# Kernel optimization log

Measured on AMD Instinct MI355X. Metric: run time of the kernel, lower is better.

The kernel has to match this reference:

```python
import jax, jax.numpy as jnp
import numpy as np

M = 16384      # total flat points per role (8 scenes x 2048 pts)
D = 256        # d_model
H = 4          # heads
K = 16         # knn neighbors
DFF = 1024     # 4*D
LN_EPS = 1e-5


def _ln(x, g, b):
    m = jnp.mean(x, axis=-1, keepdims=True)
    v = jnp.mean((x - m) ** 2, axis=-1, keepdims=True)
    return (x - m) / jnp.sqrt(v + LN_EPS) * g + b


def _knn_block(x, coord, ctx, ctx_coord, idx,
               Wq, Wk, Wv, Wo, g1, b1, pe_w, pe_b,
               W1, bf1, W2, bf2, g2, b2):
    # x: [M,D] query feats; ctx: [N,D] context feats; idx: [M,K] neighbor ids (-1 = invalid)
    m, d = x.shape
    k = idx.shape[1]
    dh = d // H
    valid = idx >= 0
    idx_c = jnp.where(valid, idx, 0)

    xn = _ln(x, g1, b1)
    q = (xn @ Wq).reshape(m, H, dh)                      # [M,H,dh]
    k_all = ctx @ Wk                                     # [N,D]
    v_all = ctx @ Wv                                     # [N,D]

    rel = coord[:, None, :] - ctx_coord[idx_c]           # [M,K,3]
    pe = rel @ pe_w + pe_b                               # [M,K,D] relative position encoding
    kg = (k_all[idx_c] + pe).reshape(m, k, H, dh)        # gathered keys  [M,K,H,dh]
    vg = (v_all[idx_c] + pe).reshape(m, k, H, dh)        # gathered values

    scale = jnp.asarray(1.0 / np.sqrt(dh), x.dtype)
    scores = jnp.einsum('mhd,mkhd->mhk', q, kg) * scale
    scores = jnp.where(valid[:, None, :], scores, jnp.asarray(-1e9, x.dtype))
    attn = jax.nn.softmax(scores, axis=-1)
    out = jnp.einsum('mhk,mkhd->mhd', attn, vg).reshape(m, d) @ Wo
    x = x + out
    h = jax.nn.gelu(_ln(x, g2, b2) @ W1 + bf1)
    return x + (h @ W2 + bf2)


def setup_inputs() -> dict:
    key = jax.random.key(0)
    ks = jax.random.split(key, 24)
    s = 0.02
    nblk = 2  # [0]=self(a), [1]=cross(a,b)
    inp = {
        'feat_a': jax.random.normal(ks[0], (M, D), jnp.float32),
        'coord_a': jax.random.normal(ks[1], (M, 3), jnp.float32),
        'feat_b': jax.random.normal(ks[2], (M, D), jnp.float32),
        'coord_b': jax.random.normal(ks[3], (M, 3), jnp.float32),
        'Wq': jax.random.normal(ks[4], (nblk, D, D), jnp.float32) * s,
        'Wk': jax.random.normal(ks[5], (nblk, D, D), jnp.float32) * s,
        'Wv': jax.random.normal(ks[6], (nblk, D, D), jnp.float32) * s,
        'Wo': jax.random.normal(ks[7], (nblk, D, D), jnp.float32) * s,
        'ln1_g': jnp.ones((nblk, D), jnp.float32),
        'ln1_b': jnp.zeros((nblk, D), jnp.float32),
        'pe_w': jax.random.normal(ks[8], (nblk, 3, D), jnp.float32) * s,
        'pe_b': jnp.zeros((nblk, D), jnp.float32),
        'ffn_w1': jax.random.normal(ks[9], (nblk, D, DFF), jnp.float32) * s,
        'ffn_b1': jnp.zeros((nblk, DFF), jnp.float32),
        'ffn_w2': jax.random.normal(ks[10], (nblk, DFF, D), jnp.float32) * s,
        'ffn_b2': jnp.zeros((nblk, D), jnp.float32),
        'ln2_g': jnp.ones((nblk, D), jnp.float32),
        'ln2_b': jnp.zeros((nblk, D), jnp.float32),
        'knn_a2a': jax.random.randint(ks[11], (M, K), 0, M, jnp.int64 if jax.config.jax_enable_x64 else jnp.int32),
        'knn_a2b': jax.random.randint(ks[12], (M, K), 0, M, jnp.int64 if jax.config.jax_enable_x64 else jnp.int32),
    }
    return inp


def reference(feat_a, coord_a, feat_b, coord_b,
              Wq, Wk, Wv, Wo, ln1_g, ln1_b, pe_w, pe_b,
              ffn_w1, ffn_b1, ffn_w2, ffn_b2, ln2_g, ln2_b,
              knn_a2a, knn_a2b):
    def params(i):
        return (Wq[i], Wk[i], Wv[i], Wo[i], ln1_g[i], ln1_b[i], pe_w[i], pe_b[i],
                ffn_w1[i], ffn_b1[i], ffn_w2[i], ffn_b2[i], ln2_g[i], ln2_b[i])
    # layer 'self(a)': feat[a] = block(feat[a], coord[a], knn_indexes['a2a'])
    fa = _knn_block(feat_a, coord_a, feat_a, coord_a, knn_a2a, *params(0))
    # layer 'cross(a,b)': feat[a] = block(query=feat[a], context=feat[b], knn_indexes['a2b'])
    fa = _knn_block(fa, coord_a, feat_b, coord_b, knn_a2b, *params(1))
    return fa
```

## Files before the change

kernel.cpp:

```cpp
#include <hip/hip_runtime.h>
#include <hip/hip_bf16.h>
#include <stdint.h>

#define MM 16384
#define DD 256
#define HH 4
#define KK 16
#define DFF_ 1024

typedef __attribute__((ext_vector_type(8))) short bf16x8;
typedef __attribute__((ext_vector_type(16))) float f32x16;
typedef __attribute__((ext_vector_type(2))) float f32x2;

__device__ __forceinline__ unsigned short f2bf(float f) {
    unsigned u = __builtin_bit_cast(unsigned, f);
    unsigned r = u + 0x7fffu + ((u >> 16) & 1u);
    return (unsigned short)(r >> 16);
}
__device__ __forceinline__ float bf2f(unsigned short h) {
    unsigned u = ((unsigned)h) << 16;
    return __builtin_bit_cast(float, u);
}


__global__ __launch_bounds__(256) void prep_weights(
        const float* __restrict__ Wq, const float* __restrict__ Wk,
        const float* __restrict__ Wv, const float* __restrict__ Wo,
        const float* __restrict__ W1, const float* __restrict__ W2,
        unsigned short* __restrict__ wf) {
    int t = blockIdx.x * blockDim.x + threadIdx.x;
    const float* src; unsigned short* dst;
    int kd, lg, rem, blk, e, sect;
    if (t < 131072) { sect = 0; rem = t; blk = rem >> 16; e = rem & 65535;
        src = Wq; dst = wf + blk * 65536; kd = 256; lg = 8; }
    else if (t < 262144) { sect = 1; rem = t - 131072; blk = rem >> 16; e = rem & 65535;
        src = Wk; dst = wf + 131072 + blk * 131072; kd = 256; lg = 8; }
    else if (t < 393216) { sect = 2; rem = t - 262144; blk = rem >> 16; e = rem & 65535;
        src = Wv; dst = wf + 131072 + blk * 131072; kd = 256; lg = 8; }
    else if (t < 524288) { sect = 0; rem = t - 393216; blk = rem >> 16; e = rem & 65535;
        src = Wo; dst = wf + 393216 + blk * 65536; kd = 256; lg = 8; }
    else if (t < 1048576) { sect = 0; rem = t - 524288; blk = rem >> 18; e = rem & 262143;
        src = W1; dst = wf + 524288 + blk * 262144; kd = 256; lg = 10; }
    else if (t < 1572864) { sect = 0; rem = t - 1048576; blk = rem >> 18; e = rem & 262143;
        src = W2; dst = wf + 1048576 + blk * 262144; kd = 1024; lg = 8; }
    else return;
    int k = e >> lg;
    int n = e & ((1 << lg) - 1);
    if (sect == 1) n = (n >> 2) * 8 + (n & 3);
    else if (sect == 2) n = (n >> 2) * 8 + 4 + (n & 3);
    float v = src[(size_t)blk * kd * (1 << lg) + e];
    int off = ((n >> 5) * (kd >> 4) + (k >> 4)) * 512 + (((k >> 3) & 1) * 32 + (n & 31)) * 8 + (k & 7);
    dst[off] = f2bf(v);
}

__global__ __launch_bounds__(256) void ln3_to_frag(
        const float* __restrict__ xa, const float* __restrict__ g,
        const float* __restrict__ b, const float* __restrict__ xb,
        unsigned short* __restrict__ outln, unsigned short* __restrict__ outca,
        unsigned short* __restrict__ outcb) {
    int y = blockIdx.y;
    const float* x = (y == 2) ? xb : xa;
    unsigned short* out = (y == 0) ? outln : (y == 1 ? outca : outcb);
    int apply_ln = (y == 0);
    int wave = threadIdx.x >> 6, lane = threadIdx.x & 63;
    int m = blockIdx.x * 4 + wave;
    const float4 xv = reinterpret_cast<const float4*>(x + (size_t)m * DD)[lane];
    float vals[4] = {xv.x, xv.y, xv.z, xv.w};
    int k0 = lane * 4;
    if (apply_ln) {
        float s = vals[0] + vals[1] + vals[2] + vals[3];
        float sq = vals[0]*vals[0] + vals[1]*vals[1] + vals[2]*vals[2] + vals[3]*vals[3];
        for (int o = 32; o; o >>= 1) { s += __shfl_xor(s, o, 64); sq += __shfl_xor(sq, o, 64); }
        float mean = s * (1.0f / DD);
        float var = sq * (1.0f / DD) - mean * mean;
        float rs = rsqrtf(var + 1e-5f);
        #pragma unroll
        for (int c = 0; c < 4; ++c)
            vals[c] = (vals[c] - mean) * rs * g[k0 + c] + b[k0 + c];
    }
    int chunk = ((m >> 5) * (DD >> 4) + (k0 >> 4)) * 64 + ((k0 >> 3) & 1) * 32 + (m & 31);
    ushort4 o4 = make_ushort4(f2bf(vals[0]), f2bf(vals[1]), f2bf(vals[2]), f2bf(vals[3]));
    *reinterpret_cast<ushort4*>(out + (size_t)chunk * 8 + (k0 & 7)) = o4;
}

constexpr int GOUT_F32 = 0;
constexpr int GOUT_GELU_FRAG = 2;

template <int KG>
__device__ __forceinline__ void compute_tile(
        const bf16x8* __restrict__ a0, const bf16x8* __restrict__ a1,
        const bf16x8* __restrict__ b0, const bf16x8* __restrict__ b1,
        f32x16 acc[2][2]) {
    #pragma unroll 4
    for (int g = 0; g < KG; ++g) {
        bf16x8 av0 = a0[g * 64];
        bf16x8 av1 = a1[g * 64];
        bf16x8 bv0 = b0[g * 64];
        bf16x8 bv1 = b1[g * 64];
        acc[0][0] = __builtin_amdgcn_mfma_f32_32x32x16_bf16(av0, bv0, acc[0][0], 0, 0, 0);
        acc[0][1] = __builtin_amdgcn_mfma_f32_32x32x16_bf16(av0, bv1, acc[0][1], 0, 0, 0);
        acc[1][0] = __builtin_amdgcn_mfma_f32_32x32x16_bf16(av1, bv0, acc[1][0], 0, 0, 0);
        acc[1][1] = __builtin_amdgcn_mfma_f32_32x32x16_bf16(av1, bv1, acc[1][1], 0, 0, 0);
    }
}

template <int KD, int NOUT, int MODE, bool RESID, bool BIAS>
__global__ __launch_bounds__(256) void gemm_frag(
        const bf16x8* __restrict__ A, const bf16x8* __restrict__ B,
        void* __restrict__ outp, const float* __restrict__ resid,
        const float* __restrict__ bias, int out_kd) {
    constexpr int KG = KD / 16;
    __shared__ float lds[MODE == GOUT_GELU_FRAG ? 4 * 1056 : 4];
    int wave = threadIdx.x >> 6, lane = threadIdx.x & 63;
    int wm = wave & 1, wn = wave >> 1;
    int m0 = blockIdx.x * 128 + wm * 64;
    int n0 = blockIdx.y * 128 + wn * 64;
    const bf16x8* a0 = A + ((size_t)(m0 >> 5) * KG) * 64 + lane;
    const bf16x8* a1 = a0 + (size_t)KG * 64;
    const bf16x8* b0 = B + ((size_t)(n0 >> 5) * KG) * 64 + lane;
    const bf16x8* b1 = b0 + (size_t)KG * 64;
    f32x16 acc[2][2] = {};
    compute_tile<KG>(a0, a1, b0, b1, acc);
    int col = lane & 31, rq = (lane >> 5) * 4;
    if constexpr (MODE == GOUT_F32) {
        #pragma unroll
        for (int i = 0; i < 2; ++i)
        #pragma unroll
        for (int j = 0; j < 2; ++j) {
            #pragma unroll
            for (int r = 0; r < 16; ++r) {
                int row = (r & 3) + 8 * (r >> 2) + rq;
                int m = m0 + i * 32 + row;
                int n = n0 + j * 32 + col;
                float v = acc[i][j][r];
                if (BIAS) v += bias[n];
                if (RESID) v += resid[(size_t)m * NOUT + n];
                ((float*)outp)[(size_t)m * NOUT + n] = v;
            }
        }
    } else {
        float* wlds = &lds[wave * 1056];
        for (int i = 0; i < 2; ++i)
        for (int j = 0; j < 2; ++j) {
            #pragma unroll
            for (int r = 0; r < 16; ++r) {
                int row = (r & 3) + 8 * (r >> 2) + rq;
                int n = n0 + j * 32 + col;
                float v = acc[i][j][r] + bias[n];
                float arg = v * (1.5957691216f + 0.0713548163f * v * v);
                v = v * __frcp_rn(1.0f + __expf(-arg));
                wlds[row * 33 + col] = v;
            }
            #pragma unroll
            for (int it = 0; it < 2; ++it) {
                int task = lane + it * 64;
                int row = task >> 2, cc = task & 3;
                int m = m0 + i * 32 + row;
                int k = n0 + j * 32 + cc * 8;
                float* p = &wlds[row * 33 + cc * 8];
                unsigned short us[8];
                #pragma unroll
                for (int e = 0; e < 8; ++e) us[e] = f2bf(p[e]);
                int chunk = ((m >> 5) * (out_kd >> 4) + (k >> 4)) * 64 + ((k >> 3) & 1) * 32 + (m & 31);
                reinterpret_cast<uint4*>(outp)[chunk] = *reinterpret_cast<uint4*>(us);
            }
        }
    }
}

template <int O, int N>
__device__ __forceinline__ void redstage(float* a, int lane) {
    int sel = lane & O;
    #pragma unroll
    for (int u = 0; u < N / 2; ++u) {
        float lo = a[2 * u], hi = a[2 * u + 1];
        float keep = sel ? hi : lo;
        float send = sel ? lo : hi;
        a[u] = keep + __shfl_xor(send, O, 64);
    }
}

template <int KD, bool BIAS>
__global__ __launch_bounds__(256) void gemm_ln(
        const bf16x8* __restrict__ A, const bf16x8* __restrict__ B,
        float* __restrict__ out_f32, const float* __restrict__ resid,
        const float* __restrict__ bias,
        const float* __restrict__ lng, const float* __restrict__ lnb,
        unsigned short* __restrict__ out_frag) {
    constexpr int KG = KD / 16;
    __shared__ float pstat[4][64][2];
    __shared__ float stats[64][2];
    __shared__ float tlds[4][32 * 33];
    int wave = threadIdx.x >> 6, lane = threadIdx.x & 63;
    int wn = wave;
    int m0 = blockIdx.x * 64;
    int n0 = wn * 64;
    const bf16x8* a0 = A + ((size_t)(m0 >> 5) * KG) * 64 + lane;
    const bf16x8* a1 = a0 + (size_t)KG * 64;
    const bf16x8* b0 = B + ((size_t)(n0 >> 5) * KG) * 64 + lane;
    const bf16x8* b1 = b0 + (size_t)KG * 64;
    f32x16 acc[2][2] = {};
    compute_tile<KG>(a0, a1, b0, b1, acc);
    int col = lane & 31, rq = (lane >> 5) * 4;

    #pragma unroll
    for (int i = 0; i < 2; ++i)
    #pragma unroll
    for (int j = 0; j < 2; ++j) {
        #pragma unroll
        for (int r = 0; r < 16; ++r) {
            int row = (r & 3) + 8 * (r >> 2) + rq;
            int m = m0 + i * 32 + row;
            int n = n0 + j * 32 + col;
            float v = acc[i][j][r];
            if (BIAS) v += bias[n];
            v += resid[(size_t)m * DD + n];
            out_f32[(size_t)m * DD + n] = v;
            acc[i][j][r] = v;
        }
    }

    {
        float ps[32];
        #pragma unroll
        for (int i = 0; i < 2; ++i)
        #pragma unroll
        for (int r = 0; r < 16; ++r)
            ps[i * 16 + r] = acc[i][0][r] + acc[i][1][r];
        redstage<1, 32>(ps, lane);
        redstage<2, 16>(ps, lane);
        redstage<4, 8>(ps, lane);
        redstage<8, 4>(ps, lane);
        redstage<16, 2>(ps, lane);
        float sum64 = ps[0];
        float qs[32];
        #pragma unroll
        for (int i = 0; i < 2; ++i)
        #pragma unroll
        for (int r = 0; r < 16; ++r) {
            float a = acc[i][0][r], b = acc[i][1][r];
            qs[i * 16 + r] = a * a + b * b;
        }
        redstage<1, 32>(qs, lane);
        redstage<2, 16>(qs, lane);
        redstage<4, 8>(qs, lane);
        redstage<8, 4>(qs, lane);
        redstage<16, 2>(qs, lane);
        float sq64 = qs[0];
        int slot = lane & 31;
        int ROW = (slot >> 4) * 32 + (slot & 3) + 8 * ((slot >> 2) & 3) + rq;
        *reinterpret_cast<float2*>(&pstat[wn][ROW][0]) = make_float2(sum64, sq64);
    }
    __syncthreads();
    if (threadIdx.x < 64) {
        int R = threadIdx.x;
        float s = 0.0f, sq = 0.0f;
        #pragma unroll
        for (int w = 0; w < 4; ++w) {
            float2 p = *reinterpret_cast<float2*>(&pstat[w][R][0]);
            s += p.x; sq += p.y;
        }
        float mean = s * (1.0f / DD);
        float var = sq * (1.0f / DD) - mean * mean;
        float rstd = rsqrtf(var + 1e-5f);
        *reinterpret_cast<float2*>(&stats[R][0]) = make_float2(mean, rstd);
    }
    __syncthreads();

    float* wlds = &tlds[wave][0];
    #pragma unroll
    for (int i = 0; i < 2; ++i) {
        float mean_r[16], rstd_r[16];
        #pragma unroll
        for (int r = 0; r < 16; ++r) {
            int row = (r & 3) + 8 * (r >> 2) + rq;
            float2 st = *reinterpret_cast<float2*>(&stats[i * 32 + row][0]);
            mean_r[r] = st.x; rstd_r[r] = st.y;
        }
        for (int j = 0; j < 2; ++j) {
            float gj = lng[n0 + j * 32 + col];
            float bj = lnb[n0 + j * 32 + col];
            #pragma unroll
            for (int r = 0; r < 16; ++r) {
                int row = (r & 3) + 8 * (r >> 2) + rq;
                float v = (acc[i][j][r] - mean_r[r]) * rstd_r[r] * gj + bj;
                wlds[row * 33 + col] = v;
            }
            #pragma unroll
            for (int it = 0; it < 2; ++it) {
                int task = lane + it * 64;
                int row = task >> 2, cc = task & 3;
                int m = m0 + i * 32 + row;
                int k = n0 + j * 32 + cc * 8;
                float* p = &wlds[row * 33 + cc * 8];
                unsigned short us[8];
                #pragma unroll
                for (int e = 0; e < 8; ++e) us[e] = f2bf(p[e]);
                int chunk = ((m >> 5) * (DD >> 4) + (k >> 4)) * 64 + ((k >> 3) & 1) * 32 + (m & 31);
                *reinterpret_cast<uint4*>(out_frag + (size_t)chunk * 8) = *reinterpret_cast<uint4*>(us);
            }
        }
    }
}

__global__ __launch_bounds__(256) void gemm_qkv(
        const bf16x8* __restrict__ Aq, const bf16x8* __restrict__ Akv,
        const bf16x8* __restrict__ Bq, const bf16x8* __restrict__ Bkv,
        unsigned short* __restrict__ qout, unsigned char* __restrict__ kvout) {
    constexpr int KG = 16;
    int wave = threadIdx.x >> 6, lane = threadIdx.x & 63;
    int wm = wave & 1, wn = wave >> 1;
    int y = blockIdx.y;
    bool isQ = y < 2;
    const bf16x8* A = isQ ? Aq : Akv;
    const bf16x8* B = isQ ? Bq : Bkv;
    int n0 = (isQ ? y : y - 2) * 128 + wn * 64;
    int m0 = blockIdx.x * 128 + wm * 64;
    const bf16x8* a0 = A + ((size_t)(m0 >> 5) * KG) * 64 + lane;
    const bf16x8* a1 = a0 + (size_t)KG * 64;
    const bf16x8* b0 = B + ((size_t)(n0 >> 5) * KG) * 64 + lane;
    const bf16x8* b1 = b0 + (size_t)KG * 64;
    f32x16 acc[2][2] = {};
    compute_tile<KG>(a0, a1, b0, b1, acc);
    int col = lane & 31, rq = (lane >> 5) * 4;
    #pragma unroll
    for (int i = 0; i < 2; ++i)
    #pragma unroll
    for (int j = 0; j < 2; ++j)
    #pragma unroll
    for (int r = 0; r < 16; ++r) {
        int row = (r & 3) + 8 * (r >> 2) + rq;
        int m = m0 + i * 32 + row;
        int n = n0 + j * 32 + col;
        float v = acc[i][j][r];
        if (isQ) qout[(size_t)m * 256 + n] = f2bf(v);
        else kvout[(size_t)m * 512 + n] =
            (unsigned char)(__builtin_amdgcn_cvt_pk_fp8_f32(v, v, 0, false) & 0xff);
    }
}

__global__ __launch_bounds__(256) void attn_kernel(
        const unsigned short* __restrict__ q, const unsigned char* __restrict__ kv,
        const float* __restrict__ coord, const float* __restrict__ ctx_coord,
        const int* __restrict__ knn,
        const float* __restrict__ pe_w, const float* __restrict__ pe_b,
        unsigned short* __restrict__ out_frag) {
    int wave = threadIdx.x >> 6, lane = threadIdx.x & 63;
    int m = blockIdx.x * 4 + wave;
    int s = lane & 15;
    int d0 = (lane >> 4) * 64 + s * 4;

    ushort4 qv4 = *reinterpret_cast<const ushort4*>(q + (size_t)m * DD + d0);
    float qx = bf2f(qv4.x), qy = bf2f(qv4.y), qz = bf2f(qv4.z), qw = bf2f(qv4.w);
    float4 pw0 = *reinterpret_cast<const float4*>(pe_w + d0);
    float4 pw1 = *reinterpret_cast<const float4*>(pe_w + DD + d0);
    float4 pw2 = *reinterpret_cast<const float4*>(pe_w + 2 * DD + d0);
    float4 pbv = *reinterpret_cast<const float4*>(pe_b + d0);

    float cx = coord[m * 3], cy = coord[m * 3 + 1], cz = coord[m * 3 + 2];
    int myidx = knn[(size_t)m * KK + s];
    int icm = myidx < 0 ? 0 : myidx;
    float rx = cx - ctx_coord[icm * 3];
    float ry = cy - ctx_coord[icm * 3 + 1];
    float rz = cz - ctx_coord[icm * 3 + 2];

    float t0 = qx * pw0.x + qy * pw0.y + qz * pw0.z + qw * pw0.w;
    float t1 = qx * pw1.x + qy * pw1.y + qz * pw1.z + qw * pw1.w;
    float t2 = qx * pw2.x + qy * pw2.y + qz * pw2.z + qw * pw2.w;
    float t3 = qx * pbv.x + qy * pbv.y + qz * pbv.z + qw * pbv.w;
    #pragma unroll
    for (int o = 1; o < 16; o <<= 1) {
        t0 += __shfl_xor(t0, o, 64);
        t1 += __shfl_xor(t1, o, 64);
        t2 += __shfl_xor(t2, o, 64);
        t3 += __shfl_xor(t3, o, 64);
    }

    float sc_own = 0.0f;
    unsigned vpk[KK];
    #pragma unroll
    for (int j = 0; j < KK; ++j) {
        int ij = __shfl(myidx, j, 64);
        int ic = ij < 0 ? 0 : ij;
        uint2 kvv = *reinterpret_cast<const uint2*>(kv + (size_t)ic * 512 + (d0 >> 2) * 8);
        vpk[j] = kvv.y;
        f32x2 k01 = __builtin_amdgcn_cvt_pk_f32_fp8(kvv.x, false);
        f32x2 k23 = __builtin_amdgcn_cvt_pk_f32_fp8(kvv.x, true);
        float p = qx * k01.x + qy * k01.y + qz * k23.x + qw * k23.y;
        p += __shfl_xor(p, 1, 64);
        p += __shfl_xor(p, 2, 64);
        p += __shfl_xor(p, 4, 64);
        p += __shfl_xor(p, 8, 64);
        sc_own = (j == s) ? p : sc_own;
    }
    float corr = rx * t0 + ry * t1 + rz * t2 + t3;
    sc_own = (myidx >= 0) ? (sc_own + corr) * 0.125f : -1e9f;

    float mx = sc_own;
    mx = fmaxf(mx, __shfl_xor(mx, 1, 64));
    mx = fmaxf(mx, __shfl_xor(mx, 2, 64));
    mx = fmaxf(mx, __shfl_xor(mx, 4, 64));
    mx = fmaxf(mx, __shfl_xor(mx, 8, 64));
    float e = __expf(sc_own - mx);
    float sum = e;
    sum += __shfl_xor(sum, 1, 64);
    sum += __shfl_xor(sum, 2, 64);
    sum += __shfl_xor(sum, 4, 64);
    sum += __shfl_xor(sum, 8, 64);
    float w_own = e * __frcp_rn(sum);

    float wrx = w_own * rx, wry = w_own * ry, wrz = w_own * rz;
    #pragma unroll
    for (int o = 1; o < 16; o <<= 1) {
        wrx += __shfl_xor(wrx, o, 64);
        wry += __shfl_xor(wry, o, 64);
        wrz += __shfl_xor(wrz, o, 64);
    }

    int gbase = lane & 48;
    float ax = 0.f, ay = 0.f, az = 0.f, aw = 0.f;
    #pragma unroll
    for (int j = 0; j < KK; ++j) {
        float wj = __shfl(w_own, gbase + j, 64);
        f32x2 v01 = __builtin_amdgcn_cvt_pk_f32_fp8(vpk[j], false);
        f32x2 v23 = __builtin_amdgcn_cvt_pk_f32_fp8(vpk[j], true);
        ax += wj * v01.x;
        ay += wj * v01.y;
        az += wj * v23.x;
        aw += wj * v23.y;
    }
    ax += wrx * pw0.x + wry * pw1.x + wrz * pw2.x + pbv.x;
    ay += wrx * pw0.y + wry * pw1.y + wrz * pw2.y + pbv.y;
    az += wrx * pw0.z + wry * pw1.z + wrz * pw2.z + pbv.z;
    aw += wrx * pw0.w + wry * pw1.w + wrz * pw2.w + pbv.w;

    ushort4 o4 = make_ushort4(f2bf(ax), f2bf(ay), f2bf(az), f2bf(aw));
    int chunk = ((m >> 5) * (DD >> 4) + (d0 >> 4)) * 64 + ((d0 >> 3) & 1) * 32 + (m & 31);
    *reinterpret_cast<ushort4*>(out_frag + (size_t)chunk * 8 + (d0 & 7)) = o4;
}

extern "C" void kernel_launch(void* const* d_in, const int* in_sizes, int n_in,
                              void* d_out, int out_size, void* d_ws, size_t ws_size,
                              hipStream_t stream) {
    const float* feat_a = (const float*)d_in[0];
    const float* coord_a = (const float*)d_in[1];
    const float* feat_b = (const float*)d_in[2];
    const float* coord_b = (const float*)d_in[3];
    const float* Wq = (const float*)d_in[4];
    const float* Wk = (const float*)d_in[5];
    const float* Wv = (const float*)d_in[6];
    const float* Wo = (const float*)d_in[7];
    const float* ln1_g = (const float*)d_in[8];
    const float* ln1_b = (const float*)d_in[9];
    const float* pe_w = (const float*)d_in[10];
    const float* pe_b = (const float*)d_in[11];
    const float* W1 = (const float*)d_in[12];
    const float* b1 = (const float*)d_in[13];
    const float* W2 = (const float*)d_in[14];
    const float* b2 = (const float*)d_in[15];
    const float* ln2_g = (const float*)d_in[16];
    const float* ln2_b = (const float*)d_in[17];
    const int* knn_a2a = (const int*)d_in[18];
    const int* knn_a2b = (const int*)d_in[19];

    char* ws = (char*)d_ws;
    unsigned short* wfrag = (unsigned short*)ws;
    float* xmid = (float*)(ws + (4ull << 20));
    float* xout0 = (float*)(ws + (20ull << 20));
    unsigned short* qbuf = (unsigned short*)(ws + (36ull << 20));
    unsigned char* kvbuf = (unsigned char*)(ws + (52ull << 20));
    unsigned short* xnf = (unsigned short*)(ws + (68ull << 20));
    unsigned short* ctxfa = (unsigned short*)(ws + (76ull << 20));
    unsigned short* attnf = (unsigned short*)(ws + (84ull << 20));
    unsigned short* ctxfb = (unsigned short*)(ws + (92ull << 20));
    unsigned short* geluf = (unsigned short*)(ws + (36ull << 20));

    const unsigned short* WQF = wfrag;
    const unsigned short* KVF = wfrag + 131072;
    const unsigned short* WOF = wfrag + 393216;
    const unsigned short* W1F = wfrag + 524288;
    const unsigned short* W2F = wfrag + 1048576;

    prep_weights<<<(1572864 + 255) / 256, 256, 0, stream>>>(Wq, Wk, Wv, Wo, W1, W2, wfrag);

    ln3_to_frag<<<dim3(MM / 4, 3), 256, 0, stream>>>(feat_a, ln1_g, ln1_b, feat_b,
                                                     xnf, ctxfa, ctxfb);

    gemm_qkv<<<dim3(MM / 128, 6), 256, 0, stream>>>(
        (const bf16x8*)xnf, (const bf16x8*)ctxfa,
        (const bf16x8*)WQF, (const bf16x8*)KVF, qbuf, kvbuf);

    attn_kernel<<<MM / 4, 256, 0, stream>>>(qbuf, kvbuf, coord_a, coord_a, knn_a2a,
                                            pe_w, pe_b, attnf);

    gemm_ln<256, false><<<MM / 64, 256, 0, stream>>>(
        (const bf16x8*)attnf, (const bf16x8*)WOF, xmid, feat_a, nullptr,
        ln2_g, ln2_b, xnf);

    gemm_frag<256, 1024, GOUT_GELU_FRAG, false, true><<<dim3(MM / 128, 8), 256, 0, stream>>>(
        (const bf16x8*)xnf, (const bf16x8*)W1F, geluf, nullptr, b1, 1024);

    gemm_ln<1024, true><<<MM / 64, 256, 0, stream>>>(
        (const bf16x8*)geluf, (const bf16x8*)W2F, xout0, xmid, b2,
        ln1_g + DD, ln1_b + DD, xnf);

    gemm_qkv<<<dim3(MM / 128, 6), 256, 0, stream>>>(
        (const bf16x8*)xnf, (const bf16x8*)ctxfb,
        (const bf16x8*)(WQF + 65536), (const bf16x8*)(KVF + 131072), qbuf, kvbuf);

    attn_kernel<<<MM / 4, 256, 0, stream>>>(qbuf, kvbuf, coord_a, coord_b, knn_a2b,
                                            pe_w + 3 * DD, pe_b + DD, attnf);

    gemm_ln<256, false><<<MM / 64, 256, 0, stream>>>(
        (const bf16x8*)attnf, (const bf16x8*)(WOF + 65536), xmid, xout0, nullptr,
        ln2_g + DD, ln2_b + DD, xnf);

    gemm_frag<256, 1024, GOUT_GELU_FRAG, false, true><<<dim3(MM / 128, 8), 256, 0, stream>>>(
        (const bf16x8*)xnf, (const bf16x8*)(W1F + 262144), geluf, nullptr,
        b1 + DFF_, 1024);

    gemm_frag<1024, 256, GOUT_F32, true, true><<<dim3(MM / 128, 2), 256, 0, stream>>>(
        (const bf16x8*)geluf, (const bf16x8*)(W2F + 262144), d_out, xmid,
        b2 + DD, 0);
}
```

Before: 335.7 us.

## Stage GEMM operand tiles into LDS via global_load_lds before MFMA

Replaces direct per-wave global fragment loads in the QKV, FFN1 and final FFN2 GEMMs with block-wide staging of A and B tiles into 128KB of shared memory using global_load_lds. The four waves then read shared data, so each global fragment is fetched once per block instead of once per wave. This removes duplicated global traffic, but the large LDS allocation limits occupancy to one block per CU. Load and compute are not overlapped within a chunk, since a full vmcnt wait and barrier come before each compute.

```diff
diff --git a/kernel.cpp b/kernel.cpp
--- a/kernel.cpp
+++ b/kernel.cpp
@@ -20,6 +20,12 @@
 __device__ __forceinline__ float bf2f(unsigned short h) {
     unsigned u = ((unsigned)h) << 16;
     return __builtin_bit_cast(float, u);
+}
+
+__device__ __forceinline__ void gload_lds16(const void* g, void* l) {
+    __builtin_amdgcn_global_load_lds(
+        (const __attribute__((address_space(1))) unsigned int*)g,
+        (__attribute__((address_space(3))) unsigned int*)l, 16, 0, 0);
 }
 
 
@@ -104,23 +110,53 @@
     }
 }
 
+template <int KG, int KGC>
+__device__ __forceinline__ void stage_tile(
+        const char* __restrict__ A, const char* __restrict__ B,
+        int m0, int n0, int c, char* smem, int wave, int lane) {
+    #pragma unroll
+    for (int r = 0; r < 32; ++r) {
+        int off = (wave + 4 * r) << 10;
+        const char* gsrc;
+        if (off < 65536) {
+            int grp = off >> 14, inner = off & 16383;
+            gsrc = A + (((size_t)((m0 >> 5) + grp) * KG + (size_t)c * KGC) << 10) + inner;
+        } else {
+            int o2 = off - 65536;
+            int grp = o2 >> 14, inner = o2 & 16383;
+            gsrc = B + (((size_t)((n0 >> 5) + grp) * KG + (size_t)c * KGC) << 10) + inner;
+        }
+        gload_lds16(gsrc + lane * 16, smem + off);
+    }
+}
+
 template <int KD, int NOUT, int MODE, bool RESID, bool BIAS>
-__global__ __launch_bounds__(256) void gemm_frag(
-        const bf16x8* __restrict__ A, const bf16x8* __restrict__ B,
+__global__ __launch_bounds__(256) void gemm_staged(
+        const char* __restrict__ A, const char* __restrict__ B,
         void* __restrict__ outp, const float* __restrict__ resid,
         const float* __restrict__ bias, int out_kd) {
     constexpr int KG = KD / 16;
-    __shared__ float lds[MODE == GOUT_GELU_FRAG ? 4 * 1056 : 4];
+    constexpr int KGC = 16;
+    constexpr int NCH = KG / KGC;
+    __shared__ char smem[131072];
     int wave = threadIdx.x >> 6, lane = threadIdx.x & 63;
     int wm = wave & 1, wn = wave >> 1;
-    int m0 = blockIdx.x * 128 + wm * 64;
-    int n0 = blockIdx.y * 128 + wn * 64;
-    const bf16x8* a0 = A + ((size_t)(m0 >> 5) * KG) * 64 + lane;
-    const bf16x8* a1 = a0 + (size_t)KG * 64;
-    const bf16x8* b0 = B + ((size_t)(n0 >> 5) * KG) * 64 + lane;
-    const bf16x8* b1 = b0 + (size_t)KG * 64;
+    int m0 = blockIdx.x * 128;
+    int n0 = blockIdx.y * 128;
+    const bf16x8* la0 = (const bf16x8*)smem + (2 * wm * KGC) * 64 + lane;
+    const bf16x8* la1 = la0 + KGC * 64;
+    const bf16x8* lb0 = (const bf16x8*)(smem + 65536) + (2 * wn * KGC) * 64 + lane;
+    const bf16x8* lb1 = lb0 + KGC * 64;
     f32x16 acc[2][2] = {};
-    compute_tile<KG>(a0, a1, b0, b1, acc);
+    #pragma unroll
+    for (int c = 0; c < NCH; ++c) {
+        if (c) __syncthreads();
+        stage_tile<KG, KGC>(A, B, m0, n0, c, smem, wave, lane);
+        asm volatile("s_waitcnt vmcnt(0)" ::: "memory");
+        __syncthreads();
+        compute_tile<KGC>(la0, la1, lb0, lb1, acc);
+    }
+    int mw = m0 + wm * 64, nw = n0 + wn * 64;
     int col = lane & 31, rq = (lane >> 5) * 4;
     if constexpr (MODE == GOUT_F32) {
         #pragma unroll
@@ -130,8 +166,8 @@
             #pragma unroll
             for (int r = 0; r < 16; ++r) {
                 int row = (r & 3) + 8 * (r >> 2) + rq;
-                int m = m0 + i * 32 + row;
-                int n = n0 + j * 32 + col;
+                int m = mw + i * 32 + row;
+                int n = nw + j * 32 + col;
                 float v = acc[i][j][r];
                 if (BIAS) v += bias[n];
                 if (RESID) v += resid[(size_t)m * NOUT + n];
@@ -139,13 +175,14 @@
             }
         }
     } else {
-        float* wlds = &lds[wave * 1056];
+        __syncthreads();
+        float* wlds = (float*)smem + wave * 1056;
         for (int i = 0; i < 2; ++i)
         for (int j = 0; j < 2; ++j) {
             #pragma unroll
             for (int r = 0; r < 16; ++r) {
                 int row = (r & 3) + 8 * (r >> 2) + rq;
-                int n = n0 + j * 32 + col;
+                int n = nw + j * 32 + col;
                 float v = acc[i][j][r] + bias[n];
                 float arg = v * (1.5957691216f + 0.0713548163f * v * v);
                 v = v * __frcp_rn(1.0f + __expf(-arg));
@@ -155,8 +192,8 @@
             for (int it = 0; it < 2; ++it) {
                 int task = lane + it * 64;
                 int row = task >> 2, cc = task & 3;
-                int m = m0 + i * 32 + row;
-                int k = n0 + j * 32 + cc * 8;
+                int m = mw + i * 32 + row;
+                int k = nw + j * 32 + cc * 8;
                 float* p = &wlds[row * 33 + cc * 8];
                 unsigned short us[8];
                 #pragma unroll
@@ -165,6 +202,47 @@
                 reinterpret_cast<uint4*>(outp)[chunk] = *reinterpret_cast<uint4*>(us);
             }
         }
+    }
+}
+
+__global__ __launch_bounds__(256) void gemm_qkv_st(
+        const char* __restrict__ Aq, const char* __restrict__ Akv,
+        const char* __restrict__ Bq, const char* __restrict__ Bkv,
+        unsigned short* __restrict__ qout, unsigned char* __restrict__ kvout) {
+    constexpr int KG = 16;
+    __shared__ char smem[131072];
+    int wave = threadIdx.x >> 6, lane = threadIdx.x & 63;
+    int wm = wave & 1, wn = wave >> 1;
+    int y = blockIdx.y;
+    bool isQ = y < 2;
+    const char* A = isQ ? Aq : Akv;
+    const char* B = isQ ? Bq : Bkv;
+    int m0 = blockIdx.x * 128;
+    int n0 = (isQ ? y : y - 2) * 128;
+    stage_tile<KG, KG>(A, B, m0, n0, 0, smem, wave, lane);
+    const bf16x8* la0 = (const bf16x8*)smem + (2 * wm * KG) * 64 + lane;
+    const bf16x8* la1 = la0 + KG * 64;
+    const bf16x8* lb0 = (const bf16x8*)(smem + 65536) + (2 * wn * KG) * 64 + lane;
+    const bf16x8* lb1 = lb0 + KG * 64;
+    f32x16 acc[2][2] = {};
+    asm volatile("s_waitcnt vmcnt(0)" ::: "memory");
+    __syncthreads();
+    compute_tile<KG>(la0, la1, lb0, lb1, acc);
+    int mw = m0 + wm * 64, nw = n0 + wn * 64;
+    int col = lane & 31, rq = (lane >> 5) * 4;
+    #pragma unroll
+    for (int i = 0; i < 2; ++i)
+    #pragma unroll
+    for (int j = 0; j < 2; ++j)
+    #pragma unroll
+    for (int r = 0; r < 16; ++r) {
+        int row = (r & 3) + 8 * (r >> 2) + rq;
+        int m = mw + i * 32 + row;
+        int n = nw + j * 32 + col;
+        float v = acc[i][j][r];
+        if (isQ) qout[(size_t)m * 256 + n] = f2bf(v);
+        else kvout[(size_t)m * 512 + n] =
+            (unsigned char)(__builtin_amdgcn_cvt_pk_fp8_f32(v, v, 0, false) & 0xff);
     }
 }
 
@@ -300,42 +378,6 @@
                 *reinterpret_cast<uint4*>(out_frag + (size_t)chunk * 8) = *reinterpret_cast<uint4*>(us);
             }
         }
-    }
-}
-
-__global__ __launch_bounds__(256) void gemm_qkv(
-        const bf16x8* __restrict__ Aq, const bf16x8* __restrict__ Akv,
-        const bf16x8* __restrict__ Bq, const bf16x8* __restrict__ Bkv,
-        unsigned short* __restrict__ qout, unsigned char* __restrict__ kvout) {
-    constexpr int KG = 16;
-    int wave = threadIdx.x >> 6, lane = threadIdx.x & 63;
-    int wm = wave & 1, wn = wave >> 1;
-    int y = blockIdx.y;
-    bool isQ = y < 2;
-    const bf16x8* A = isQ ? Aq : Akv;
-    const bf16x8* B = isQ ? Bq : Bkv;
-    int n0 = (isQ ? y : y - 2) * 128 + wn * 64;
-    int m0 = blockIdx.x * 128 + wm * 64;
-    const bf16x8* a0 = A + ((size_t)(m0 >> 5) * KG) * 64 + lane;
-    const bf16x8* a1 = a0 + (size_t)KG * 64;
-    const bf16x8* b0 = B + ((size_t)(n0 >> 5) * KG) * 64 + lane;
-    const bf16x8* b1 = b0 + (size_t)KG * 64;
-    f32x16 acc[2][2] = {};
-    compute_tile<KG>(a0, a1, b0, b1, acc);
-    int col = lane & 31, rq = (lane >> 5) * 4;
-    #pragma unroll
-    for (int i = 0; i < 2; ++i)
-    #pragma unroll
-    for (int j = 0; j < 2; ++j)
-    #pragma unroll
-    for (int r = 0; r < 16; ++r) {
-        int row = (r & 3) + 8 * (r >> 2) + rq;
-        int m = m0 + i * 32 + row;
-        int n = n0 + j * 32 + col;
-        float v = acc[i][j][r];
-        if (isQ) qout[(size_t)m * 256 + n] = f2bf(v);
-        else kvout[(size_t)m * 512 + n] =
-            (unsigned char)(__builtin_amdgcn_cvt_pk_fp8_f32(v, v, 0, false) & 0xff);
     }
 }
 
@@ -486,9 +528,9 @@
     ln3_to_frag<<<dim3(MM / 4, 3), 256, 0, stream>>>(feat_a, ln1_g, ln1_b, feat_b,
                                                      xnf, ctxfa, ctxfb);
 
-    gemm_qkv<<<dim3(MM / 128, 6), 256, 0, stream>>>(
-        (const bf16x8*)xnf, (const bf16x8*)ctxfa,
-        (const bf16x8*)WQF, (const bf16x8*)KVF, qbuf, kvbuf);
+    gemm_qkv_st<<<dim3(MM / 128, 6), 256, 0, stream>>>(
+        (const char*)xnf, (const char*)ctxfa,
+        (const char*)WQF, (const char*)KVF, qbuf, kvbuf);
 
     attn_kernel<<<MM / 4, 256, 0, stream>>>(qbuf, kvbuf, coord_a, coord_a, knn_a2a,
                                             pe_w, pe_b, attnf);
@@ -497,16 +539,16 @@
         (const bf16x8*)attnf, (const bf16x8*)WOF, xmid, feat_a, nullptr,
         ln2_g, ln2_b, xnf);
 
-    gemm_frag<256, 1024, GOUT_GELU_FRAG, false, true><<<dim3(MM / 128, 8), 256, 0, stream>>>(
-        (const bf16x8*)xnf, (const bf16x8*)W1F, geluf, nullptr, b1, 1024);
+    gemm_staged<256, 1024, GOUT_GELU_FRAG, false, true><<<dim3(MM / 128, 8), 256, 0, stream>>>(
+        (const char*)xnf, (const char*)W1F, geluf, nullptr, b1, 1024);
 
     gemm_ln<1024, true><<<MM / 64, 256, 0, stream>>>(
         (const bf16x8*)geluf, (const bf16x8*)W2F, xout0, xmid, b2,
         ln1_g + DD, ln1_b + DD, xnf);
 
-    gemm_qkv<<<dim3(MM / 128, 6), 256, 0, stream>>>(
-        (const bf16x8*)xnf, (const bf16x8*)ctxfb,
-        (const bf16x8*)(WQF + 65536), (const bf16x8*)(KVF + 131072), qbuf, kvbuf);
+    gemm_qkv_st<<<dim3(MM / 128, 6), 256, 0, stream>>>(
+        (const char*)xnf, (const char*)ctxfb,
+        (const char*)(WQF + 65536), (const char*)(KVF + 131072), qbuf, kvbuf);
 
     attn_kernel<<<MM / 4, 256, 0, stream>>>(qbuf, kvbuf, coord_a, coord_b, knn_a2b,
                                             pe_w + 3 * DD, pe_b + DD, attnf);
@@ -515,11 +557,11 @@
         (const bf16x8*)attnf, (const bf16x8*)(WOF + 65536), xmid, xout0, nullptr,
         ln2_g + DD, ln2_b + DD, xnf);
 
-    gemm_frag<256, 1024, GOUT_GELU_FRAG, false, true><<<dim3(MM / 128, 8), 256, 0, stream>>>(
-        (const bf16x8*)xnf, (const bf16x8*)(W1F + 262144), geluf, nullptr,
+    gemm_staged<256, 1024, GOUT_GELU_FRAG, false, true><<<dim3(MM / 128, 8), 256, 0, stream>>>(
+        (const char*)xnf, (const char*)(W1F + 262144), geluf, nullptr,
         b1 + DFF_, 1024);
 
-    gemm_frag<1024, 256, GOUT_F32, true, true><<<dim3(MM / 128, 2), 256, 0, stream>>>(
-        (const bf16x8*)geluf, (const bf16x8*)(W2F + 262144), d_out, xmid,
+    gemm_staged<1024, 256, GOUT_F32, true, true><<<dim3(MM / 128, 2), 256, 0, stream>>>(
+        (const char*)geluf, (const char*)(W2F + 262144), d_out, xmid,
         b2 + DD, 0);
 }
```

Measured after the change: 368.7 us. 1.1x slower.

## Split GEMM+LN tiles across 8 waves, add 64-row final GEMM, batch attention score reductions

Applied to the files above, without the earlier changes.

The fused GEMM+LayerNorm kernel now runs 512 threads with 8 waves, each computing a 32x64 tile instead of 64x64. This halves the per-wave accumulator registers and adds more waves per block for latency hiding. The last FFN down-projection moves to a new 64-row-tile GEMM so the grid has more blocks. In attention, the 16 per-neighbor butterfly shuffle reductions become a transpose-style redstage reduction that uses fewer shuffles. The trade-off is more blocks re-reading the same B fragments and a different reduction pattern.

```diff
diff --git a/kernel.cpp b/kernel.cpp
--- a/kernel.cpp
+++ b/kernel.cpp
@@ -168,137 +168,40 @@
     }
 }
 
-template <int O, int N>
-__device__ __forceinline__ void redstage(float* a, int lane) {
-    int sel = lane & O;
-    #pragma unroll
-    for (int u = 0; u < N / 2; ++u) {
-        float lo = a[2 * u], hi = a[2 * u + 1];
-        float keep = sel ? hi : lo;
-        float send = sel ? lo : hi;
-        a[u] = keep + __shfl_xor(send, O, 64);
-    }
-}
-
-template <int KD, bool BIAS>
-__global__ __launch_bounds__(256) void gemm_ln(
+template <int KD, int NOUT, bool RESID, bool BIAS>
+__global__ __launch_bounds__(256) void gemm_frag64(
         const bf16x8* __restrict__ A, const bf16x8* __restrict__ B,
-        float* __restrict__ out_f32, const float* __restrict__ resid,
-        const float* __restrict__ bias,
-        const float* __restrict__ lng, const float* __restrict__ lnb,
-        unsigned short* __restrict__ out_frag) {
+        float* __restrict__ outp, const float* __restrict__ resid,
+        const float* __restrict__ bias) {
     constexpr int KG = KD / 16;
-    __shared__ float pstat[4][64][2];
-    __shared__ float stats[64][2];
-    __shared__ float tlds[4][32 * 33];
     int wave = threadIdx.x >> 6, lane = threadIdx.x & 63;
-    int wn = wave;
-    int m0 = blockIdx.x * 64;
-    int n0 = wn * 64;
-    const bf16x8* a0 = A + ((size_t)(m0 >> 5) * KG) * 64 + lane;
-    const bf16x8* a1 = a0 + (size_t)KG * 64;
-    const bf16x8* b0 = B + ((size_t)(n0 >> 5) * KG) * 64 + lane;
+    int wm = wave & 1, wn = wave >> 1;
+    int mw = blockIdx.x * 64 + wm * 32;
+    int nw = blockIdx.y * 128 + wn * 64;
+    const bf16x8* a0 = A + ((size_t)(mw >> 5) * KG) * 64 + lane;
+    const bf16x8* b0 = B + ((size_t)(nw >> 5) * KG) * 64 + lane;
     const bf16x8* b1 = b0 + (size_t)KG * 64;
-    f32x16 acc[2][2] = {};
-    compute_tile<KG>(a0, a1, b0, b1, acc);
+    f32x16 acc[2] = {};
+    #pragma unroll 4
+    for (int g = 0; g < KG; ++g) {
+        bf16x8 av = a0[g * 64];
+        bf16x8 bv0 = b0[g * 64];
+        bf16x8 bv1 = b1[g * 64];
+        acc[0] = __builtin_amdgcn_mfma_f32_32x32x16_bf16(av, bv0, acc[0], 0, 0, 0);
+        acc[1] = __builtin_amdgcn_mfma_f32_32x32x16_bf16(av, bv1, acc[1], 0, 0, 0);
+    }
     int col = lane & 31, rq = (lane >> 5) * 4;
-
-    #pragma unroll
-    for (int i = 0; i < 2; ++i)
     #pragma unroll
     for (int j = 0; j < 2; ++j) {
         #pragma unroll
         for (int r = 0; r < 16; ++r) {
             int row = (r & 3) + 8 * (r >> 2) + rq;
-            int m = m0 + i * 32 + row;
-            int n = n0 + j * 32 + col;
-            float v = acc[i][j][r];
+            int m = mw + row;
+            int n = nw + j * 32 + col;
+            float v = acc[j][r];
             if (BIAS) v += bias[n];
-            v += resid[(size_t)m * DD + n];
-            out_f32[(size_t)m * DD + n] = v;
-            acc[i][j][r] = v;
-        }
-    }
-
-    {
-        float ps[32];
-        #pragma unroll
-        for (int i = 0; i < 2; ++i)
-        #pragma unroll
-        for (int r = 0; r < 16; ++r)
-            ps[i * 16 + r] = acc[i][0][r] + acc[i][1][r];
-        redstage<1, 32>(ps, lane);
-        redstage<2, 16>(ps, lane);
-        redstage<4, 8>(ps, lane);
-        redstage<8, 4>(ps, lane);
-        redstage<16, 2>(ps, lane);
-        float sum64 = ps[0];
-        float qs[32];
-        #pragma unroll
-        for (int i = 0; i < 2; ++i)
-        #pragma unroll
-        for (int r = 0; r < 16; ++r) {
-            float a = acc[i][0][r], b = acc[i][1][r];
-            qs[i * 16 + r] = a * a + b * b;
-        }
-        redstage<1, 32>(qs, lane);
-        redstage<2, 16>(qs, lane);
-        redstage<4, 8>(qs, lane);
-        redstage<8, 4>(qs, lane);
-        redstage<16, 2>(qs, lane);
-        float sq64 = qs[0];
-        int slot = lane & 31;
-        int ROW = (slot >> 4) * 32 + (slot & 3) + 8 * ((slot >> 2) & 3) + rq;
-        *reinterpret_cast<float2*>(&pstat[wn][ROW][0]) = make_float2(sum64, sq64);
-    }
-    __syncthreads();
-    if (threadIdx.x < 64) {
-        int R = threadIdx.x;
-        float s = 0.0f, sq = 0.0f;
-        #pragma unroll
-        for (int w = 0; w < 4; ++w) {
-            float2 p = *reinterpret_cast<float2*>(&pstat[w][R][0]);
-            s += p.x; sq += p.y;
-        }
-        float mean = s * (1.0f / DD);
-        float var = sq * (1.0f / DD) - mean * mean;
-        float rstd = rsqrtf(var + 1e-5f);
-        *reinterpret_cast<float2*>(&stats[R][0]) = make_float2(mean, rstd);
-    }
-    __syncthreads();
-
-    float* wlds = &tlds[wave][0];
-    #pragma unroll
-    for (int i = 0; i < 2; ++i) {
-        float mean_r[16], rstd_r[16];
-        #pragma unroll
-        for (int r = 0; r < 16; ++r) {
-            int row = (r & 3) + 8 * (r >> 2) + rq;
-            float2 st = *reinterpret_cast<float2*>(&stats[i * 32 + row][0]);
-            mean_r[r] = st.x; rstd_r[r] = st.y;
-        }
-        for (int j = 0; j < 2; ++j) {
-            float gj = lng[n0 + j * 32 + col];
-            float bj = lnb[n0 + j * 32 + col];
-            #pragma unroll
-            for (int r = 0; r < 16; ++r) {
-                int row = (r & 3) + 8 * (r >> 2) + rq;
-                float v = (acc[i][j][r] - mean_r[r]) * rstd_r[r] * gj + bj;
-                wlds[row * 33 + col] = v;
-            }
-            #pragma unroll
-            for (int it = 0; it < 2; ++it) {
-                int task = lane + it * 64;
-                int row = task >> 2, cc = task & 3;
-                int m = m0 + i * 32 + row;
-                int k = n0 + j * 32 + cc * 8;
-                float* p = &wlds[row * 33 + cc * 8];
-                unsigned short us[8];
-                #pragma unroll
-                for (int e = 0; e < 8; ++e) us[e] = f2bf(p[e]);
-                int chunk = ((m >> 5) * (DD >> 4) + (k >> 4)) * 64 + ((k >> 3) & 1) * 32 + (m & 31);
-                *reinterpret_cast<uint4*>(out_frag + (size_t)chunk * 8) = *reinterpret_cast<uint4*>(us);
-            }
+            if (RESID) v += resid[(size_t)m * NOUT + n];
+            outp[(size_t)m * NOUT + n] = v;
         }
     }
 }
@@ -339,6 +242,138 @@
     }
 }
 
+template <int O, int N>
+__device__ __forceinline__ void redstage(float* a, int lane) {
+    int sel = lane & O;
+    #pragma unroll
+    for (int u = 0; u < N / 2; ++u) {
+        float lo = a[2 * u], hi = a[2 * u + 1];
+        float keep = sel ? hi : lo;
+        float send = sel ? lo : hi;
+        a[u] = keep + __shfl_xor(send, O, 64);
+    }
+}
+
+template <int KD, bool BIAS>
+__global__ __launch_bounds__(512) void gemm_ln(
+        const bf16x8* __restrict__ A, const bf16x8* __restrict__ B,
+        float* __restrict__ out_f32, const float* __restrict__ resid,
+        const float* __restrict__ bias,
+        const float* __restrict__ lng, const float* __restrict__ lnb,
+        unsigned short* __restrict__ out_frag) {
+    constexpr int KG = KD / 16;
+    __shared__ float pstat[4][64][2];
+    __shared__ float stats[64][2];
+    __shared__ float tlds[8][32 * 33];
+    int wave = threadIdx.x >> 6, lane = threadIdx.x & 63;
+    int wm = wave >> 2, wn = wave & 3;
+    int m0 = blockIdx.x * 64;
+    int mw = m0 + wm * 32;
+    int n0 = wn * 64;
+    const bf16x8* a0 = A + ((size_t)(mw >> 5) * KG) * 64 + lane;
+    const bf16x8* b0 = B + ((size_t)(n0 >> 5) * KG) * 64 + lane;
+    const bf16x8* b1 = b0 + (size_t)KG * 64;
+    f32x16 acc[2] = {};
+    #pragma unroll 4
+    for (int g = 0; g < KG; ++g) {
+        bf16x8 av = a0[g * 64];
+        bf16x8 bv0 = b0[g * 64];
+        bf16x8 bv1 = b1[g * 64];
+        acc[0] = __builtin_amdgcn_mfma_f32_32x32x16_bf16(av, bv0, acc[0], 0, 0, 0);
+        acc[1] = __builtin_amdgcn_mfma_f32_32x32x16_bf16(av, bv1, acc[1], 0, 0, 0);
+    }
+    int col = lane & 31, rq = (lane >> 5) * 4;
+
+    #pragma unroll
+    for (int j = 0; j < 2; ++j) {
+        #pragma unroll
+        for (int r = 0; r < 16; ++r) {
+            int row = (r & 3) + 8 * (r >> 2) + rq;
+            int m = mw + row;
+            int n = n0 + j * 32 + col;
+            float v = acc[j][r];
+            if (BIAS) v += bias[n];
+            v += resid[(size_t)m * DD + n];
+            out_f32[(size_t)m * DD + n] = v;
+            acc[j][r] = v;
+        }
+    }
+
+    {
+        float ps[16];
+        #pragma unroll
+        for (int r = 0; r < 16; ++r)
+            ps[r] = acc[0][r] + acc[1][r];
+        redstage<1, 16>(ps, lane);
+        redstage<2, 8>(ps, lane);
+        redstage<4, 4>(ps, lane);
+        redstage<8, 2>(ps, lane);
+        float sum64 = ps[0] + __shfl_xor(ps[0], 16, 64);
+        float qs[16];
+        #pragma unroll
+        for (int r = 0; r < 16; ++r) {
+            float a = acc[0][r], b = acc[1][r];
+            qs[r] = a * a + b * b;
+        }
+        redstage<1, 16>(qs, lane);
+        redstage<2, 8>(qs, lane);
+        redstage<4, 4>(qs, lane);
+        redstage<8, 2>(qs, lane);
+        float sq64 = qs[0] + __shfl_xor(qs[0], 16, 64);
+        int slot = lane & 15;
+        int ROW = wm * 32 + (slot & 3) + 8 * (slot >> 2) + rq;
+        if ((lane & 16) == 0)
+            *reinterpret_cast<float2*>(&pstat[wn][ROW][0]) = make_float2(sum64, sq64);
+    }
+    __syncthreads();
+    if (threadIdx.x < 64) {
+        int R = threadIdx.x;
+        float s = 0.0f, sq = 0.0f;
+        #pragma unroll
+        for (int w = 0; w < 4; ++w) {
+            float2 p = *reinterpret_cast<float2*>(&pstat[w][R][0]);
+            s += p.x; sq += p.y;
+        }
+        float mean = s * (1.0f / DD);
+        float var = sq * (1.0f / DD) - mean * mean;
+        float rstd = rsqrtf(var + 1e-5f);
+        *reinterpret_cast<float2*>(&stats[R][0]) = make_float2(mean, rstd);
+    }
+    __syncthreads();
+
+    float* wlds = &tlds[wave][0];
+    float mean_r[16], rstd_r[16];
+    #pragma unroll
+    for (int r = 0; r < 16; ++r) {
+        int row = (r & 3) + 8 * (r >> 2) + rq;
+        float2 st = *reinterpret_cast<float2*>(&stats[wm * 32 + row][0]);
+        mean_r[r] = st.x; rstd_r[r] = st.y;
+    }
+    for (int j = 0; j < 2; ++j) {
+        float gj = lng[n0 + j * 32 + col];
+        float bj = lnb[n0 + j * 32 + col];
+        #pragma unroll
+        for (int r = 0; r < 16; ++r) {
+            int row = (r & 3) + 8 * (r >> 2) + rq;
+            float v = (acc[j][r] - mean_r[r]) * rstd_r[r] * gj + bj;
+            wlds[row * 33 + col] = v;
+        }
+        #pragma unroll
+        for (int it = 0; it < 2; ++it) {
+            int task = lane + it * 64;
+            int row = task >> 2, cc = task & 3;
+            int m = mw + row;
+            int k = n0 + j * 32 + cc * 8;
+            float* p = &wlds[row * 33 + cc * 8];
+            unsigned short us[8];
+            #pragma unroll
+            for (int e = 0; e < 8; ++e) us[e] = f2bf(p[e]);
+            int chunk = ((m >> 5) * (DD >> 4) + (k >> 4)) * 64 + ((k >> 3) & 1) * 32 + (m & 31);
+            *reinterpret_cast<uint4*>(out_frag + (size_t)chunk * 8) = *reinterpret_cast<uint4*>(us);
+        }
+    }
+}
+
 __global__ __launch_bounds__(256) void attn_kernel(
         const unsigned short* __restrict__ q, const unsigned char* __restrict__ kv,
         const float* __restrict__ coord, const float* __restrict__ ctx_coord,
@@ -376,7 +411,7 @@
         t3 += __shfl_xor(t3, o, 64);
     }
 
-    float sc_own = 0.0f;
+    float P[KK];
     unsigned vpk[KK];
     #pragma unroll
     for (int j = 0; j < KK; ++j) {
@@ -386,15 +421,14 @@
         vpk[j] = kvv.y;
         f32x2 k01 = __builtin_amdgcn_cvt_pk_f32_fp8(kvv.x, false);
         f32x2 k23 = __builtin_amdgcn_cvt_pk_f32_fp8(kvv.x, true);
-        float p = qx * k01.x + qy * k01.y + qz * k23.x + qw * k23.y;
-        p += __shfl_xor(p, 1, 64);
-        p += __shfl_xor(p, 2, 64);
-        p += __shfl_xor(p, 4, 64);
-        p += __shfl_xor(p, 8, 64);
-        sc_own = (j == s) ? p : sc_own;
-    }
+        P[j] = qx * k01.x + qy * k01.y + qz * k23.x + qw * k23.y;
+    }
+    redstage<1, 16>(P, lane);
+    redstage<2, 8>(P, lane);
+    redstage<4, 4>(P, lane);
+    redstage<8, 2>(P, lane);
     float corr = rx * t0 + ry * t1 + rz * t2 + t3;
-    sc_own = (myidx >= 0) ? (sc_own + corr) * 0.125f : -1e9f;
+    float sc_own = (myidx >= 0) ? (P[0] + corr) * 0.125f : -1e9f;
 
     float mx = sc_own;
     mx = fmaxf(mx, __shfl_xor(mx, 1, 64));
@@ -493,14 +527,14 @@
     attn_kernel<<<MM / 4, 256, 0, stream>>>(qbuf, kvbuf, coord_a, coord_a, knn_a2a,
                                             pe_w, pe_b, attnf);
 
-    gemm_ln<256, false><<<MM / 64, 256, 0, stream>>>(
+    gemm_ln<256, false><<<MM / 64, 512, 0, stream>>>(
         (const bf16x8*)attnf, (const bf16x8*)WOF, xmid, feat_a, nullptr,
         ln2_g, ln2_b, xnf);
 
     gemm_frag<256, 1024, GOUT_GELU_FRAG, false, true><<<dim3(MM / 128, 8), 256, 0, stream>>>(
         (const bf16x8*)xnf, (const bf16x8*)W1F, geluf, nullptr, b1, 1024);
 
-    gemm_ln<1024, true><<<MM / 64, 256, 0, stream>>>(
+    gemm_ln<1024, true><<<MM / 64, 512, 0, stream>>>(
         (const bf16x8*)geluf, (const bf16x8*)W2F, xout0, xmid, b2,
         ln1_g + DD, ln1_b + DD, xnf);
 
@@ -511,7 +545,7 @@
     attn_kernel<<<MM / 4, 256, 0, stream>>>(qbuf, kvbuf, coord_a, coord_b, knn_a2b,
                                             pe_w + 3 * DD, pe_b + DD, attnf);
 
-    gemm_ln<256, false><<<MM / 64, 256, 0, stream>>>(
+    gemm_ln<256, false><<<MM / 64, 512, 0, stream>>>(
         (const bf16x8*)attnf, (const bf16x8*)(WOF + 65536), xmid, xout0, nullptr,
         ln2_g + DD, ln2_b + DD, xnf);
 
@@ -519,7 +553,7 @@
         (const bf16x8*)xnf, (const bf16x8*)(W1F + 262144), geluf, nullptr,
         b1 + DFF_, 1024);
 
-    gemm_frag<1024, 256, GOUT_F32, true, true><<<dim3(MM / 128, 2), 256, 0, stream>>>(
-        (const bf16x8*)geluf, (const bf16x8*)(W2F + 262144), d_out, xmid,
-        b2 + DD, 0);
-}
+    gemm_frag64<1024, 256, true, true><<<dim3(MM / 64, 2), 256, 0, stream>>>(
+        (const bf16x8*)geluf, (const bf16x8*)(W2F + 262144), (float*)d_out, xmid,
+        b2 + DD);
+}
```

Result: faster. 311.8 us (-7.1%).
